# Kernel optimization log

Measured on AMD Instinct MI355X. Metric: run time of the kernel, lower is better.

The kernel has to match this reference:

```python
import jax, jax.numpy as jnp
import numpy as np

N = 100_000      # nodes
E = 1_600_000    # edges (avg degree 16)
IN, H, OUT = 128, 64, 32
G = 128          # graphs in batch
EPS = 1e-5


def setup_inputs() -> dict:
    key = jax.random.key(0)
    ks = jax.random.split(key, 12)
    x = jax.random.normal(ks[0], (N, IN), jnp.float32)
    edge_index = jax.random.randint(ks[1], (2, E), 0, N, dtype=jnp.int32)
    batch = jnp.sort(jax.random.randint(ks[2], (N,), 0, G, dtype=jnp.int32))
    # GCNConv weights (glorot-ish scaling), shared BatchNorm params, final linear
    W1 = jax.random.normal(ks[3], (IN, H), jnp.float32) / np.sqrt(IN)
    b1 = jnp.zeros((H,), jnp.float32)
    W2 = jax.random.normal(ks[4], (H, H), jnp.float32) / np.sqrt(H)
    b2 = jnp.zeros((H,), jnp.float32)
    gamma = jnp.ones((H,), jnp.float32)
    beta = jnp.zeros((H,), jnp.float32)
    linW = jax.random.normal(ks[5], (H, OUT), jnp.float32) / np.sqrt(H)
    linb = jnp.zeros((OUT,), jnp.float32)
    return dict(x=x, edge_index=edge_index, batch=batch, W1=W1, b1=b1,
                W2=W2, b2=b2, gamma=gamma, beta=beta, linW=linW, linb=linb)


def _gcn_edges(edge_index):
    # add self loops (PyG GCNConv default) and symmetric normalization
    loop = jnp.arange(N, dtype=edge_index.dtype)
    src = jnp.concatenate([edge_index[0], loop])
    dst = jnp.concatenate([edge_index[1], loop])
    deg = jax.ops.segment_sum(jnp.ones_like(src, jnp.float32), dst, num_segments=N)
    dis = jnp.where(deg > 0, jax.lax.rsqrt(deg), 0.0)
    norm = dis[src] * dis[dst]          # [E+N]
    return src, dst, norm


def _gcn_conv(h, W, b, src, dst, norm):
    h = h @ W                            # [N, out] small GEMM first (PyG order)
    msg = h[src] * norm[:, None]         # gather + edgewise normalize
    return jax.ops.segment_sum(msg, dst, num_segments=N) + b  # scatter-add


def _batchnorm(h, gamma, beta):
    # training-mode batch stats over nodes (biased variance, as torch BN)
    mean = h.mean(axis=0)
    var = jnp.mean((h - mean) ** 2, axis=0)
    return (h - mean) * jax.lax.rsqrt(var + EPS) * gamma + beta


def reference(x, edge_index, batch, W1, b1, W2, b2, gamma, beta, linW, linb):
    src, dst, norm = _gcn_edges(edge_index)
    h = jax.nn.relu(_batchnorm(_gcn_conv(x, W1, b1, src, dst, norm), gamma, beta))
    h = jax.nn.relu(_batchnorm(_gcn_conv(h, W2, b2, src, dst, norm), gamma, beta))
    # global mean pool over graph ids
    sums = jax.ops.segment_sum(h, batch, num_segments=G)
    cnts = jax.ops.segment_sum(jnp.ones((N,), h.dtype), batch, num_segments=G)
    pooled = sums / jnp.maximum(cnts, 1.0)[:, None]   # [G, H]
    return pooled @ linW + linb                        # [G, OUT]
```

## Files before the change

kernel.cpp:

```cpp
#include <hip/hip_runtime.h>

#define NNODES 100000
#define NEDGES 1600000
#define FIN 128
#define FH 64
#define FOUT 32
#define NGRAPH 128
#define EPSV 1e-5f

#define SCAN_BT 256
#define NBLK ((NNODES + SCAN_BT - 1) / SCAN_BT)

typedef unsigned short ushort_t;
typedef __attribute__((ext_vector_type(8))) short bf16x8;
typedef __attribute__((ext_vector_type(4))) float f32x4;

__device__ inline unsigned f2bf(float f) {
  union { float f; unsigned u; } x;
  x.f = f;
  return (x.u + 0x7fffu + ((x.u >> 16) & 1u)) >> 16;
}
__device__ inline float bflo(unsigned u) {
  union { unsigned u; float f; } x;
  x.u = u << 16;
  return x.f;
}
__device__ inline float bfhi(unsigned u) {
  union { unsigned u; float f; } x;
  x.u = u & 0xffff0000u;
  return x.f;
}


__global__ void k_init_deg(float* __restrict__ deg) {
  int i = blockIdx.x * blockDim.x + threadIdx.x;
  if (i < NNODES) deg[i] = 1.0f;
}

__global__ void k_deg_accum(const int* __restrict__ dst, float* __restrict__ deg) {
  int i = blockIdx.x * blockDim.x + threadIdx.x;
  if (i < NEDGES) atomicAdd(&deg[dst[i]], 1.0f);
}

__global__ void k_rsqrt(float* __restrict__ deg) {
  int i = blockIdx.x * blockDim.x + threadIdx.x;
  if (i < NNODES) deg[i] = rsqrtf(deg[i]);
}


__global__ void k_blocksum(const float* __restrict__ deg, int* __restrict__ bsum) {
  __shared__ int ls[SCAN_BT];
  int b = blockIdx.x, t = threadIdx.x;
  int i = b * SCAN_BT + t;
  ls[t] = (i < NNODES) ? (int)deg[i] - 1 : 0;
  __syncthreads();
  for (int s = SCAN_BT / 2; s > 0; s >>= 1) {
    if (t < s) ls[t] += ls[t + s];
    __syncthreads();
  }
  if (t == 0) bsum[b] = ls[0];
}

__global__ void k_scan_bsums(const int* __restrict__ bsum, int* __restrict__ boff) {
  __shared__ int ls[512];
  int t = threadIdx.x;
  int v = (t < NBLK) ? bsum[t] : 0;
  ls[t] = v;
  __syncthreads();
  for (int s = 1; s < 512; s <<= 1) {
    int add = (t >= s) ? ls[t - s] : 0;
    __syncthreads();
    ls[t] += add;
    __syncthreads();
  }
  if (t < NBLK) boff[t] = ls[t] - v;
}

__global__ void k_scan_final(const float* __restrict__ deg, const int* __restrict__ boff,
                             int* __restrict__ off) {
  __shared__ int ls[SCAN_BT];
  int b = blockIdx.x, t = threadIdx.x;
  int i = b * SCAN_BT + t;
  int v = (i < NNODES) ? (int)deg[i] - 1 : 0;
  ls[t] = v;
  __syncthreads();
  for (int s = 1; s < SCAN_BT; s <<= 1) {
    int add = (t >= s) ? ls[t - s] : 0;
    __syncthreads();
    ls[t] += add;
    __syncthreads();
  }
  if (i < NNODES) off[i] = boff[b] + ls[t] - v;
  if (i == NNODES - 1) off[NNODES] = boff[b] + ls[t];
}


__global__ void k_fill(const int* __restrict__ src, const int* __restrict__ dst,
                       const int* __restrict__ off, int* __restrict__ cursor,
                       int* __restrict__ csr) {
  const int SLICE = NNODES / 8;
  int xcd = blockIdx.x & 7;
  int lo = xcd * SLICE, hi = lo + SLICE;
  int chunk = blockIdx.x >> 3;
  int nchunk = gridDim.x >> 3;
  for (int i = chunk * blockDim.x + threadIdx.x; i < NEDGES; i += nchunk * blockDim.x) {
    int d = dst[i];
    if (d >= lo && d < hi) {
      int p = atomicAdd(&cursor[d], 1);
      csr[off[d] + p] = src[i];
    }
  }
}


template <int K, bool BN>
__global__ void k_gemm_mfma(const float* __restrict__ A, const float* __restrict__ W,
                            const float* __restrict__ scsh, const float* __restrict__ dis,
                            ushort_t* __restrict__ out) {
  const int WT = K + 8;
  __shared__ ushort_t wt[64 * (K + 8)];
  for (int idx = threadIdx.x; idx < K * 64; idx += 256) {
    int k = idx >> 6, col = idx & 63;
    wt[col * WT + k] = (ushort_t)f2bf(W[idx]);
  }
  __syncthreads();

  int wave = threadIdx.x >> 6;
  int lane = threadIdx.x & 63;
  int rrow = lane & 15;
  int g = lane >> 4;
  int row0 = (blockIdx.x * 4 + wave) * 16;
  int arow = min(row0 + rrow, NNODES - 1);
  const float* a = A + (long long)arow * K;

  f32x4 acc0 = {0.f, 0.f, 0.f, 0.f}, acc1 = acc0, acc2 = acc0, acc3 = acc0;

#pragma unroll
  for (int ks = 0; ks < K / 32; ++ks) {
    int koff = ks * 32 + g * 8;
    float4 xa = *(const float4*)(a + koff);
    float4 xb = *(const float4*)(a + koff + 4);
    float xs[8] = {xa.x, xa.y, xa.z, xa.w, xb.x, xb.y, xb.z, xb.w};
    if (BN) {
#pragma unroll
      for (int j = 0; j < 8; ++j)
        xs[j] = fmaxf(fmaf(xs[j], scsh[koff + j], scsh[K + koff + j]), 0.0f);
    }
    bf16x8 af;
#pragma unroll
    for (int j = 0; j < 8; ++j) af[j] = (short)f2bf(xs[j]);
    bf16x8 b0 = *(const bf16x8*)&wt[(0 * 16 + rrow) * WT + koff];
    bf16x8 b1 = *(const bf16x8*)&wt[(1 * 16 + rrow) * WT + koff];
    bf16x8 b2 = *(const bf16x8*)&wt[(2 * 16 + rrow) * WT + koff];
    bf16x8 b3 = *(const bf16x8*)&wt[(3 * 16 + rrow) * WT + koff];
    acc0 = __builtin_amdgcn_mfma_f32_16x16x32_bf16(af, b0, acc0, 0, 0, 0);
    acc1 = __builtin_amdgcn_mfma_f32_16x16x32_bf16(af, b1, acc1, 0, 0, 0);
    acc2 = __builtin_amdgcn_mfma_f32_16x16x32_bf16(af, b2, acc2, 0, 0, 0);
    acc3 = __builtin_amdgcn_mfma_f32_16x16x32_bf16(af, b3, acc3, 0, 0, 0);
  }

  int orow0 = row0 + g * 4;
#pragma unroll
  for (int r = 0; r < 4; ++r) {
    int orow = orow0 + r;
    if (orow < NNODES) {
      float d = dis[orow];
      ushort_t* o = out + (long long)orow * FH + rrow;
      o[0] = (ushort_t)f2bf(acc0[r] * d);
      o[16] = (ushort_t)f2bf(acc1[r] * d);
      o[32] = (ushort_t)f2bf(acc2[r] * d);
      o[48] = (ushort_t)f2bf(acc3[r] * d);
    }
  }
}


__global__ void k_gather(const ushort_t* __restrict__ hs, const int* __restrict__ csr,
                         const int* __restrict__ off, const float* __restrict__ dis,
                         float* __restrict__ out, float* __restrict__ stats) {
  __shared__ float ls[2 * FH];
  int tid = threadIdx.x;
  if (tid < 2 * FH) ls[tid] = 0.0f;
  __syncthreads();
  int lane = tid & 63;
  int g = lane >> 4;
  int i = lane & 15;
  int wid = (blockIdx.x * blockDim.x + tid) >> 6;
  int nw = (gridDim.x * blockDim.x) >> 6;
  float s1x = 0, s1y = 0, s1z = 0, s1w = 0;
  float s2x = 0, s2y = 0, s2z = 0, s2w = 0;
  for (int d = wid; d < NNODES; d += nw) {
    int b = off[d], e = off[d + 1];
    uint2 su = *(const uint2*)(hs + (long long)d * FH + i * 4);
    float ax = (g == 0) ? bflo(su.x) : 0.0f;
    float ay = (g == 0) ? bfhi(su.x) : 0.0f;
    float az = (g == 0) ? bflo(su.y) : 0.0f;
    float aw = (g == 0) ? bfhi(su.y) : 0.0f;
    int niter = (e - b + 15) >> 4;
    int last = e - 1;
    int k0 = b + g;
    for (int j = 0; j < niter; ++j) {
      int i0 = k0 + 16 * j, i1 = i0 + 4, i2 = i0 + 8, i3 = i0 + 12;
      int c0 = csr[min(i0, last)];
      int c1 = csr[min(i1, last)];
      int c2 = csr[min(i2, last)];
      int c3 = csr[min(i3, last)];
      uint2 u0 = *(const uint2*)(hs + (long long)c0 * FH + i * 4);
      uint2 u1 = *(const uint2*)(hs + (long long)c1 * FH + i * 4);
      uint2 u2 = *(const uint2*)(hs + (long long)c2 * FH + i * 4);
      uint2 u3 = *(const uint2*)(hs + (long long)c3 * FH + i * 4);
      bool k0ok = i0 <= last, k1ok = i1 <= last, k2ok = i2 <= last, k3ok = i3 <= last;
      ax += (k0ok ? bflo(u0.x) : 0.0f) + (k1ok ? bflo(u1.x) : 0.0f) +
            (k2ok ? bflo(u2.x) : 0.0f) + (k3ok ? bflo(u3.x) : 0.0f);
      ay += (k0ok ? bfhi(u0.x) : 0.0f) + (k1ok ? bfhi(u1.x) : 0.0f) +
            (k2ok ? bfhi(u2.x) : 0.0f) + (k3ok ? bfhi(u3.x) : 0.0f);
      az += (k0ok ? bflo(u0.y) : 0.0f) + (k1ok ? bflo(u1.y) : 0.0f) +
            (k2ok ? bflo(u2.y) : 0.0f) + (k3ok ? bflo(u3.y) : 0.0f);
      aw += (k0ok ? bfhi(u0.y) : 0.0f) + (k1ok ? bfhi(u1.y) : 0.0f) +
            (k2ok ? bfhi(u2.y) : 0.0f) + (k3ok ? bfhi(u3.y) : 0.0f);
    }
    ax += __shfl_xor(ax, 16); ax += __shfl_xor(ax, 32);
    ay += __shfl_xor(ay, 16); ay += __shfl_xor(ay, 32);
    az += __shfl_xor(az, 16); az += __shfl_xor(az, 32);
    aw += __shfl_xor(aw, 16); aw += __shfl_xor(aw, 32);
    float dd = dis[d];
    float ox = ax * dd, oy = ay * dd, oz = az * dd, ow = aw * dd;
    if (g == 0) {
      float4 o4 = {ox, oy, oz, ow};
      *(float4*)(out + (long long)d * FH + i * 4) = o4;
    }
    s1x += ox; s2x += ox * ox;
    s1y += oy; s2y += oy * oy;
    s1z += oz; s2z += oz * oz;
    s1w += ow; s2w += ow * ow;
  }
  if (g == 0) {
    atomicAdd(&ls[i * 4 + 0], s1x);
    atomicAdd(&ls[i * 4 + 1], s1y);
    atomicAdd(&ls[i * 4 + 2], s1z);
    atomicAdd(&ls[i * 4 + 3], s1w);
    atomicAdd(&ls[FH + i * 4 + 0], s2x);
    atomicAdd(&ls[FH + i * 4 + 1], s2y);
    atomicAdd(&ls[FH + i * 4 + 2], s2z);
    atomicAdd(&ls[FH + i * 4 + 3], s2w);
  }
  __syncthreads();
  if (tid < 2 * FH) atomicAdd(&stats[tid], ls[tid]);
}

__global__ void k_bn_finalize(const float* __restrict__ stats, const float* __restrict__ gamma,
                              const float* __restrict__ beta, float* __restrict__ scsh) {
  int f = threadIdx.x;
  if (f < FH) {
    float mean = stats[f] * (1.0f / NNODES);
    float var = stats[FH + f] * (1.0f / NNODES) - mean * mean;
    float s = gamma[f] * rsqrtf(var + EPSV);
    scsh[f] = s;
    scsh[FH + f] = beta[f] - mean * s;
  }
}


#define POOL_WAVES 1024

__global__ void k_pool(const float* __restrict__ h, const int* __restrict__ batch,
                       const float* __restrict__ scsh, float* __restrict__ pooled,
                       float* __restrict__ cnt) {
  const int CHUNK = (NNODES + POOL_WAVES - 1) / POOL_WAVES;
  int lane = threadIdx.x & 63;
  int wid = (blockIdx.x * blockDim.x + threadIdx.x) >> 6;
  int start = wid * CHUNK;
  if (start >= NNODES) return;
  int end = min(start + CHUNK, NNODES);
  float sc = scsh[lane], sh = scsh[FH + lane];
  int cur = batch[start];
  float acc = 0.0f;
  int cl = 0;
  for (int n = start; n < end; ++n) {
    int g = batch[n];
    if (g != cur) {
      atomicAdd(&pooled[cur * FH + lane], acc);
      if (lane == 0) atomicAdd(&cnt[cur], (float)cl);
      acc = 0.0f;
      cl = 0;
      cur = g;
    }
    float v = fmaf(h[(long long)n * FH + lane], sc, sh);
    acc += fmaxf(v, 0.0f);
    ++cl;
  }
  atomicAdd(&pooled[cur * FH + lane], acc);
  if (lane == 0) atomicAdd(&cnt[cur], (float)cl);
}


__global__ void k_final(const float* __restrict__ pooled, const float* __restrict__ cnt,
                        const float* __restrict__ linW, const float* __restrict__ linb,
                        float* __restrict__ out) {
  int t = blockIdx.x * blockDim.x + threadIdx.x;
  if (t >= NGRAPH * FOUT) return;
  int g = t / FOUT, o = t % FOUT;
  float inv = 1.0f / fmaxf(cnt[g], 1.0f);
  float acc = linb[o];
#pragma unroll
  for (int k = 0; k < FH; ++k) acc = fmaf(pooled[g * FH + k] * inv, linW[k * FOUT + o], acc);
  out[t] = acc;
}

extern "C" void kernel_launch(void* const* d_in, const int* in_sizes, int n_in,
                              void* d_out, int out_size, void* d_ws, size_t ws_size,
                              hipStream_t stream) {
  const float* x = (const float*)d_in[0];
  const int* edge_index = (const int*)d_in[1];
  const int* batch = (const int*)d_in[2];
  const float* W1 = (const float*)d_in[3];
  const float* W2 = (const float*)d_in[5];
  const float* gamma = (const float*)d_in[7];
  const float* beta = (const float*)d_in[8];
  const float* linW = (const float*)d_in[9];
  const float* linb = (const float*)d_in[10];
  float* out = (float*)d_out;

  const int* esrc = edge_index;
  const int* edst = edge_index + NEDGES;

  ushort_t* bufA = (ushort_t*)d_ws;
  float* bufB = (float*)d_ws + (long long)NNODES * FH;
  float* dis = bufB + (long long)NNODES * FH;
  int* off = (int*)(dis + NNODES);
  int* csr = off + (NNODES + 1);
  int* bsum = csr + NEDGES;
  int* boff = bsum + NBLK;
  int* cursor = boff + NBLK;
  float* stats1 = (float*)(cursor + NNODES);
  float* scsh1 = stats1 + 2 * FH;
  float* stats2 = scsh1 + 2 * FH;
  float* scsh2 = stats2 + 2 * FH;
  float* pooled = scsh2 + 2 * FH;
  float* cnt = pooled + NGRAPH * FH;

  const int BT = 256;
  const int gN = (NNODES + BT - 1) / BT;
  const int gE = (NEDGES + BT - 1) / BT;
  const int gM = (NNODES + 63) / 64;

  hipMemsetAsync(cursor, 0,
                 (size_t)(NNODES + 4 * 2 * FH + NGRAPH * FH + NGRAPH) * sizeof(float), stream);

  k_init_deg<<<gN, BT, 0, stream>>>(dis);
  k_deg_accum<<<gE, BT, 0, stream>>>(edst, dis);
  k_blocksum<<<NBLK, SCAN_BT, 0, stream>>>(dis, bsum);
  k_scan_bsums<<<1, 512, 0, stream>>>(bsum, boff);
  k_scan_final<<<NBLK, SCAN_BT, 0, stream>>>(dis, boff, off);
  k_rsqrt<<<gN, BT, 0, stream>>>(dis);
  k_fill<<<2048, BT, 0, stream>>>(esrc, edst, off, cursor, csr);

  k_gemm_mfma<FIN, false><<<gM, BT, 0, stream>>>(x, W1, nullptr, dis, bufA);
  k_gather<<<2048, BT, 0, stream>>>(bufA, csr, off, dis, bufB, stats1);
  k_bn_finalize<<<1, 64, 0, stream>>>(stats1, gamma, beta, scsh1);

  k_gemm_mfma<FH, true><<<gM, BT, 0, stream>>>(bufB, W2, scsh1, dis, bufA);
  k_gather<<<2048, BT, 0, stream>>>(bufA, csr, off, dis, bufB, stats2);
  k_bn_finalize<<<1, 64, 0, stream>>>(stats2, gamma, beta, scsh2);

  k_pool<<<POOL_WAVES * 64 / BT, BT, 0, stream>>>(bufB, batch, scsh2, pooled, cnt);
  k_final<<<(NGRAPH * FOUT + BT - 1) / BT, BT, 0, stream>>>(pooled, cnt, linW, linb, out);
}
```

Before: 445.9 us.

## Fuse degree/rsqrt and BN finalize into neighbors; gather two nodes per wave

Degree counting now uses int atomics partitioned by XCD slice, and the rsqrt is folded into the scan-final kernel, removing the init and rsqrt kernels. The BN finalize kernels are dropped: each GEMM block and each pool wave recomputes scale and shift from the stats. The gather kernel processes two nodes per wave (p and p+HALF) to raise memory-level parallelism for the neighbor loads. Together these cut kernel launches at the cost of redundant BN math and higher register pressure in the gather.

```diff
diff --git a/kernel.cpp b/kernel.cpp
--- a/kernel.cpp
+++ b/kernel.cpp
@@ -32,27 +32,24 @@
 }
 
 
-__global__ void k_init_deg(float* __restrict__ deg) {
-  int i = blockIdx.x * blockDim.x + threadIdx.x;
-  if (i < NNODES) deg[i] = 1.0f;
-}
-
-__global__ void k_deg_accum(const int* __restrict__ dst, float* __restrict__ deg) {
-  int i = blockIdx.x * blockDim.x + threadIdx.x;
-  if (i < NEDGES) atomicAdd(&deg[dst[i]], 1.0f);
-}
-
-__global__ void k_rsqrt(float* __restrict__ deg) {
-  int i = blockIdx.x * blockDim.x + threadIdx.x;
-  if (i < NNODES) deg[i] = rsqrtf(deg[i]);
-}
-
-
-__global__ void k_blocksum(const float* __restrict__ deg, int* __restrict__ bsum) {
+__global__ void k_deg_accum(const int* __restrict__ dst, int* __restrict__ deg) {
+  const int SLICE = NNODES / 8;
+  int xcd = blockIdx.x & 7;
+  int lo = xcd * SLICE, hi = lo + SLICE;
+  int chunk = blockIdx.x >> 3;
+  int nchunk = gridDim.x >> 3;
+  for (int i = chunk * blockDim.x + threadIdx.x; i < NEDGES; i += nchunk * blockDim.x) {
+    int d = dst[i];
+    if (d >= lo && d < hi) atomicAdd(&deg[d], 1);
+  }
+}
+
+
+__global__ void k_blocksum(const int* __restrict__ deg, int* __restrict__ bsum) {
   __shared__ int ls[SCAN_BT];
   int b = blockIdx.x, t = threadIdx.x;
   int i = b * SCAN_BT + t;
-  ls[t] = (i < NNODES) ? (int)deg[i] - 1 : 0;
+  ls[t] = (i < NNODES) ? deg[i] : 0;
   __syncthreads();
   for (int s = SCAN_BT / 2; s > 0; s >>= 1) {
     if (t < s) ls[t] += ls[t + s];
@@ -76,12 +73,13 @@
   if (t < NBLK) boff[t] = ls[t] - v;
 }
 
-__global__ void k_scan_final(const float* __restrict__ deg, const int* __restrict__ boff,
-                             int* __restrict__ off) {
+
+__global__ void k_scan_final(const int* __restrict__ deg, const int* __restrict__ boff,
+                             int* __restrict__ off, float* __restrict__ dis) {
   __shared__ int ls[SCAN_BT];
   int b = blockIdx.x, t = threadIdx.x;
   int i = b * SCAN_BT + t;
-  int v = (i < NNODES) ? (int)deg[i] - 1 : 0;
+  int v = (i < NNODES) ? deg[i] : 0;
   ls[t] = v;
   __syncthreads();
   for (int s = 1; s < SCAN_BT; s <<= 1) {
@@ -90,7 +88,10 @@
     ls[t] += add;
     __syncthreads();
   }
-  if (i < NNODES) off[i] = boff[b] + ls[t] - v;
+  if (i < NNODES) {
+    off[i] = boff[b] + ls[t] - v;
+    dis[i] = rsqrtf((float)v + 1.0f);
+  }
   if (i == NNODES - 1) off[NNODES] = boff[b] + ls[t];
 }
 
@@ -115,10 +116,20 @@
 
 template <int K, bool BN>
 __global__ void k_gemm_mfma(const float* __restrict__ A, const float* __restrict__ W,
-                            const float* __restrict__ scsh, const float* __restrict__ dis,
+                            const float* __restrict__ stats, const float* __restrict__ gamma,
+                            const float* __restrict__ beta, const float* __restrict__ dis,
                             ushort_t* __restrict__ out) {
   const int WT = K + 8;
   __shared__ ushort_t wt[64 * (K + 8)];
+  __shared__ float bn_sc[K], bn_sh[K];
+  if (BN && threadIdx.x < K) {
+    int f = threadIdx.x;
+    float mean = stats[f] * (1.0f / NNODES);
+    float var = stats[K + f] * (1.0f / NNODES) - mean * mean;
+    float s = gamma[f] * rsqrtf(var + EPSV);
+    bn_sc[f] = s;
+    bn_sh[f] = beta[f] - mean * s;
+  }
   for (int idx = threadIdx.x; idx < K * 64; idx += 256) {
     int k = idx >> 6, col = idx & 63;
     wt[col * WT + k] = (ushort_t)f2bf(W[idx]);
@@ -144,7 +155,7 @@
     if (BN) {
 #pragma unroll
       for (int j = 0; j < 8; ++j)
-        xs[j] = fmaxf(fmaf(xs[j], scsh[koff + j], scsh[K + koff + j]), 0.0f);
+        xs[j] = fmaxf(fmaf(xs[j], bn_sc[koff + j], bn_sh[koff + j]), 0.0f);
     }
     bf16x8 af;
 #pragma unroll
@@ -187,52 +198,89 @@
   int i = lane & 15;
   int wid = (blockIdx.x * blockDim.x + tid) >> 6;
   int nw = (gridDim.x * blockDim.x) >> 6;
+  const int HALF = NNODES / 2;
   float s1x = 0, s1y = 0, s1z = 0, s1w = 0;
   float s2x = 0, s2y = 0, s2z = 0, s2w = 0;
-  for (int d = wid; d < NNODES; d += nw) {
-    int b = off[d], e = off[d + 1];
-    uint2 su = *(const uint2*)(hs + (long long)d * FH + i * 4);
-    float ax = (g == 0) ? bflo(su.x) : 0.0f;
-    float ay = (g == 0) ? bfhi(su.x) : 0.0f;
-    float az = (g == 0) ? bflo(su.y) : 0.0f;
-    float aw = (g == 0) ? bfhi(su.y) : 0.0f;
-    int niter = (e - b + 15) >> 4;
-    int last = e - 1;
-    int k0 = b + g;
+  for (int p = wid; p < HALF; p += nw) {
+    int dA = p, dB = p + HALF;
+    int bA = off[dA], eA = off[dA + 1];
+    int bB = off[dB], eB = off[dB + 1];
+    uint2 suA = *(const uint2*)(hs + (long long)dA * FH + i * 4);
+    uint2 suB = *(const uint2*)(hs + (long long)dB * FH + i * 4);
+    float axA = (g == 0) ? bflo(suA.x) : 0.0f;
+    float ayA = (g == 0) ? bfhi(suA.x) : 0.0f;
+    float azA = (g == 0) ? bflo(suA.y) : 0.0f;
+    float awA = (g == 0) ? bfhi(suA.y) : 0.0f;
+    float axB = (g == 0) ? bflo(suB.x) : 0.0f;
+    float ayB = (g == 0) ? bfhi(suB.x) : 0.0f;
+    float azB = (g == 0) ? bflo(suB.y) : 0.0f;
+    float awB = (g == 0) ? bfhi(suB.y) : 0.0f;
+    int nA = (eA - bA + 15) >> 4, nB = (eB - bB + 15) >> 4;
+    int niter = max(nA, nB);
+    int lastA = max(eA - 1, 0), lastB = max(eB - 1, 0);
+    int kA = bA + g, kB = bB + g;
     for (int j = 0; j < niter; ++j) {
-      int i0 = k0 + 16 * j, i1 = i0 + 4, i2 = i0 + 8, i3 = i0 + 12;
-      int c0 = csr[min(i0, last)];
-      int c1 = csr[min(i1, last)];
-      int c2 = csr[min(i2, last)];
-      int c3 = csr[min(i3, last)];
-      uint2 u0 = *(const uint2*)(hs + (long long)c0 * FH + i * 4);
-      uint2 u1 = *(const uint2*)(hs + (long long)c1 * FH + i * 4);
-      uint2 u2 = *(const uint2*)(hs + (long long)c2 * FH + i * 4);
-      uint2 u3 = *(const uint2*)(hs + (long long)c3 * FH + i * 4);
-      bool k0ok = i0 <= last, k1ok = i1 <= last, k2ok = i2 <= last, k3ok = i3 <= last;
-      ax += (k0ok ? bflo(u0.x) : 0.0f) + (k1ok ? bflo(u1.x) : 0.0f) +
-            (k2ok ? bflo(u2.x) : 0.0f) + (k3ok ? bflo(u3.x) : 0.0f);
-      ay += (k0ok ? bfhi(u0.x) : 0.0f) + (k1ok ? bfhi(u1.x) : 0.0f) +
-            (k2ok ? bfhi(u2.x) : 0.0f) + (k3ok ? bfhi(u3.x) : 0.0f);
-      az += (k0ok ? bflo(u0.y) : 0.0f) + (k1ok ? bflo(u1.y) : 0.0f) +
-            (k2ok ? bflo(u2.y) : 0.0f) + (k3ok ? bflo(u3.y) : 0.0f);
-      aw += (k0ok ? bfhi(u0.y) : 0.0f) + (k1ok ? bfhi(u1.y) : 0.0f) +
-            (k2ok ? bfhi(u2.y) : 0.0f) + (k3ok ? bfhi(u3.y) : 0.0f);
-    }
-    ax += __shfl_xor(ax, 16); ax += __shfl_xor(ax, 32);
-    ay += __shfl_xor(ay, 16); ay += __shfl_xor(ay, 32);
-    az += __shfl_xor(az, 16); az += __shfl_xor(az, 32);
-    aw += __shfl_xor(aw, 16); aw += __shfl_xor(aw, 32);
-    float dd = dis[d];
-    float ox = ax * dd, oy = ay * dd, oz = az * dd, ow = aw * dd;
-    if (g == 0) {
-      float4 o4 = {ox, oy, oz, ow};
+      int a0 = kA + 16 * j, a1 = a0 + 4, a2 = a0 + 8, a3 = a0 + 12;
+      int b0 = kB + 16 * j, b1 = b0 + 4, b2 = b0 + 8, b3 = b0 + 12;
+      int cA0 = csr[min(a0, lastA)];
+      int cA1 = csr[min(a1, lastA)];
+      int cA2 = csr[min(a2, lastA)];
+      int cA3 = csr[min(a3, lastA)];
+      int cB0 = csr[min(b0, lastB)];
+      int cB1 = csr[min(b1, lastB)];
+      int cB2 = csr[min(b2, lastB)];
+      int cB3 = csr[min(b3, lastB)];
+      uint2 uA0 = *(const uint2*)(hs + (long long)cA0 * FH + i * 4);
+      uint2 uA1 = *(const uint2*)(hs + (long long)cA1 * FH + i * 4);
+      uint2 uA2 = *(const uint2*)(hs + (long long)cA2 * FH + i * 4);
+      uint2 uA3 = *(const uint2*)(hs + (long long)cA3 * FH + i * 4);
+      uint2 uB0 = *(const uint2*)(hs + (long long)cB0 * FH + i * 4);
+      uint2 uB1 = *(const uint2*)(hs + (long long)cB1 * FH + i * 4);
+      uint2 uB2 = *(const uint2*)(hs + (long long)cB2 * FH + i * 4);
+      uint2 uB3 = *(const uint2*)(hs + (long long)cB3 * FH + i * 4);
+      bool A0 = a0 < eA, A1 = a1 < eA, A2 = a2 < eA, A3 = a3 < eA;
+      bool B0 = b0 < eB, B1 = b1 < eB, B2 = b2 < eB, B3 = b3 < eB;
+      axA += (A0 ? bflo(uA0.x) : 0.0f) + (A1 ? bflo(uA1.x) : 0.0f) +
+             (A2 ? bflo(uA2.x) : 0.0f) + (A3 ? bflo(uA3.x) : 0.0f);
+      ayA += (A0 ? bfhi(uA0.x) : 0.0f) + (A1 ? bfhi(uA1.x) : 0.0f) +
+             (A2 ? bfhi(uA2.x) : 0.0f) + (A3 ? bfhi(uA3.x) : 0.0f);
+      azA += (A0 ? bflo(uA0.y) : 0.0f) + (A1 ? bflo(uA1.y) : 0.0f) +
+             (A2 ? bflo(uA2.y) : 0.0f) + (A3 ? bflo(uA3.y) : 0.0f);
+      awA += (A0 ? bfhi(uA0.y) : 0.0f) + (A1 ? bfhi(uA1.y) : 0.0f) +
+             (A2 ? bfhi(uA2.y) : 0.0f) + (A3 ? bfhi(uA3.y) : 0.0f);
+      axB += (B0 ? bflo(uB0.x) : 0.0f) + (B1 ? bflo(uB1.x) : 0.0f) +
+             (B2 ? bflo(uB2.x) : 0.0f) + (B3 ? bflo(uB3.x) : 0.0f);
+      ayB += (B0 ? bfhi(uB0.x) : 0.0f) + (B1 ? bfhi(uB1.x) : 0.0f) +
+             (B2 ? bfhi(uB2.x) : 0.0f) + (B3 ? bfhi(uB3.x) : 0.0f);
+      azB += (B0 ? bflo(uB0.y) : 0.0f) + (B1 ? bflo(uB1.y) : 0.0f) +
+             (B2 ? bflo(uB2.y) : 0.0f) + (B3 ? bflo(uB3.y) : 0.0f);
+      awB += (B0 ? bfhi(uB0.y) : 0.0f) + (B1 ? bfhi(uB1.y) : 0.0f) +
+             (B2 ? bfhi(uB2.y) : 0.0f) + (B3 ? bfhi(uB3.y) : 0.0f);
+    }
+    axA += __shfl_xor(axA, 16); axA += __shfl_xor(axA, 32);
+    ayA += __shfl_xor(ayA, 16); ayA += __shfl_xor(ayA, 32);
+    azA += __shfl_xor(azA, 16); azA += __shfl_xor(azA, 32);
+    awA += __shfl_xor(awA, 16); awA += __shfl_xor(awA, 32);
+    axB += __shfl_xor(axB, 16); axB += __shfl_xor(axB, 32);
+    ayB += __shfl_xor(ayB, 16); ayB += __shfl_xor(ayB, 32);
+    azB += __shfl_xor(azB, 16); azB += __shfl_xor(azB, 32);
+    awB += __shfl_xor(awB, 16); awB += __shfl_xor(awB, 32);
+    float ddA = dis[dA], ddB = dis[dB];
+    float oxA = axA * ddA, oyA = ayA * ddA, ozA = azA * ddA, owA = awA * ddA;
+    float oxB = axB * ddB, oyB = ayB * ddB, ozB = azB * ddB, owB = awB * ddB;
+    if (g < 2) {
+      int d = (g == 0) ? dA : dB;
+      float4 o4;
+      o4.x = (g == 0) ? oxA : oxB;
+      o4.y = (g == 0) ? oyA : oyB;
+      o4.z = (g == 0) ? ozA : ozB;
+      o4.w = (g == 0) ? owA : owB;
       *(float4*)(out + (long long)d * FH + i * 4) = o4;
     }
-    s1x += ox; s2x += ox * ox;
-    s1y += oy; s2y += oy * oy;
-    s1z += oz; s2z += oz * oz;
-    s1w += ow; s2w += ow * ow;
+    s1x += oxA + oxB; s2x += oxA * oxA + oxB * oxB;
+    s1y += oyA + oyB; s2y += oyA * oyA + oyB * oyB;
+    s1z += ozA + ozB; s2z += ozA * ozA + ozB * ozB;
+    s1w += owA + owB; s2w += owA * owA + owB * owB;
   }
   if (g == 0) {
     atomicAdd(&ls[i * 4 + 0], s1x);
@@ -248,23 +296,12 @@
   if (tid < 2 * FH) atomicAdd(&stats[tid], ls[tid]);
 }
 
-__global__ void k_bn_finalize(const float* __restrict__ stats, const float* __restrict__ gamma,
-                              const float* __restrict__ beta, float* __restrict__ scsh) {
-  int f = threadIdx.x;
-  if (f < FH) {
-    float mean = stats[f] * (1.0f / NNODES);
-    float var = stats[FH + f] * (1.0f / NNODES) - mean * mean;
-    float s = gamma[f] * rsqrtf(var + EPSV);
-    scsh[f] = s;
-    scsh[FH + f] = beta[f] - mean * s;
-  }
-}
-
 
 #define POOL_WAVES 1024
 
 __global__ void k_pool(const float* __restrict__ h, const int* __restrict__ batch,
-                       const float* __restrict__ scsh, float* __restrict__ pooled,
+                       const float* __restrict__ stats, const float* __restrict__ gamma,
+                       const float* __restrict__ beta, float* __restrict__ pooled,
                        float* __restrict__ cnt) {
   const int CHUNK = (NNODES + POOL_WAVES - 1) / POOL_WAVES;
   int lane = threadIdx.x & 63;
@@ -272,7 +309,10 @@
   int start = wid * CHUNK;
   if (start >= NNODES) return;
   int end = min(start + CHUNK, NNODES);
-  float sc = scsh[lane], sh = scsh[FH + lane];
+  float mean = stats[lane] * (1.0f / NNODES);
+  float var = stats[FH + lane] * (1.0f / NNODES) - mean * mean;
+  float sc = gamma[lane] * rsqrtf(var + EPSV);
+  float sh = beta[lane] - mean * sc;
   int cur = batch[start];
   float acc = 0.0f;
   int cl = 0;
@@ -331,38 +371,32 @@
   int* csr = off + (NNODES + 1);
   int* bsum = csr + NEDGES;
   int* boff = bsum + NBLK;
-  int* cursor = boff + NBLK;
+  int* deg = boff + NBLK;
+  int* cursor = deg + NNODES;
   float* stats1 = (float*)(cursor + NNODES);
-  float* scsh1 = stats1 + 2 * FH;
-  float* stats2 = scsh1 + 2 * FH;
-  float* scsh2 = stats2 + 2 * FH;
-  float* pooled = scsh2 + 2 * FH;
+  float* stats2 = stats1 + 2 * FH;
+  float* pooled = stats2 + 2 * FH;
   float* cnt = pooled + NGRAPH * FH;
 
   const int BT = 256;
   const int gN = (NNODES + BT - 1) / BT;
-  const int gE = (NEDGES + BT - 1) / BT;
   const int gM = (NNODES + 63) / 64;
 
-  hipMemsetAsync(cursor, 0,
-                 (size_t)(NNODES + 4 * 2 * FH + NGRAPH * FH + NGRAPH) * sizeof(float), stream);
-
-  k_init_deg<<<gN, BT, 0, stream>>>(dis);
-  k_deg_accum<<<gE, BT, 0, stream>>>(edst, dis);
-  k_blocksum<<<NBLK, SCAN_BT, 0, stream>>>(dis, bsum);
+  hipMemsetAsync(deg, 0,
+                 (size_t)(2 * NNODES + 2 * 2 * FH + NGRAPH * FH + NGRAPH) * sizeof(int), stream);
+
+  k_deg_accum<<<2048, BT, 0, stream>>>(edst, deg);
+  k_blocksum<<<NBLK, SCAN_BT, 0, stream>>>(deg, bsum);
   k_scan_bsums<<<1, 512, 0, stream>>>(bsum, boff);
-  k_scan_final<<<NBLK, SCAN_BT, 0, stream>>>(dis, boff, off);
-  k_rsqrt<<<gN, BT, 0, stream>>>(dis);
+  k_scan_final<<<NBLK, SCAN_BT, 0, stream>>>(deg, boff, off, dis);
   k_fill<<<2048, BT, 0, stream>>>(esrc, edst, off, cursor, csr);
 
-  k_gemm_mfma<FIN, false><<<gM, BT, 0, stream>>>(x, W1, nullptr, dis, bufA);
+  k_gemm_mfma<FIN, false><<<gM, BT, 0, stream>>>(x, W1, nullptr, nullptr, nullptr, dis, bufA);
   k_gather<<<2048, BT, 0, stream>>>(bufA, csr, off, dis, bufB, stats1);
-  k_bn_finalize<<<1, 64, 0, stream>>>(stats1, gamma, beta, scsh1);
-
-  k_gemm_mfma<FH, true><<<gM, BT, 0, stream>>>(bufB, W2, scsh1, dis, bufA);
+
+  k_gemm_mfma<FH, true><<<gM, BT, 0, stream>>>(bufB, W2, stats1, gamma, beta, dis, bufA);
   k_gather<<<2048, BT, 0, stream>>>(bufA, csr, off, dis, bufB, stats2);
-  k_bn_finalize<<<1, 64, 0, stream>>>(stats2, gamma, beta, scsh2);
-
-  k_pool<<<POOL_WAVES * 64 / BT, BT, 0, stream>>>(bufB, batch, scsh2, pooled, cnt);
+
+  k_pool<<<POOL_WAVES * 64 / BT, BT, 0, stream>>>(bufB, batch, stats2, gamma, beta, pooled, cnt);
   k_final<<<(NGRAPH * FOUT + BT - 1) / BT, BT, 0, stream>>>(pooled, cnt, linW, linb, out);
 }
```

Result: faster. 418.3 us (-6.2%).
